# Optimization experiments

Measured on AMD Instinct MI355X. Metric: run time of the kernel, lower is better.

The kernel has to match this reference:

```python
import jax, jax.numpy as jnp
import numpy as np

B, S, D, H = 4, 2048, 2048, 16
DK = D // H

def setup_inputs() -> dict:
    key = jax.random.key(0)
    ks = jax.random.split(key, 9)
    def xavier(k, shape):
        fan_in, fan_out = shape[1], shape[0]
        limit = (6.0 / (fan_in + fan_out)) ** 0.5
        return jax.random.uniform(k, shape, jnp.float32, -limit, limit)
    return {
        "x": jax.random.normal(ks[0], (B, S, D), jnp.float32),
        "Wq": xavier(ks[1], (D, D)), "bq": jnp.zeros((D,), jnp.float32),
        "Wk": xavier(ks[2], (D, D)), "bk": jnp.zeros((D,), jnp.float32),
        "Wv": xavier(ks[3], (D, D)), "bv": jnp.zeros((D,), jnp.float32),
        "Wo": xavier(ks[4], (D, D)), "bo": jnp.zeros((D,), jnp.float32),
    }

def reference(x, Wq, bq, Wk, bk, Wv, bv, Wo, bo):
    b, s, d = x.shape
    scale = DK ** 0.5
    # torch nn.Linear: y = x @ W.T + b
    def proj(W, bias):
        y = jnp.einsum('bsd,ed->bse', x, W) + bias
        return y.reshape(b, s, H, DK).transpose(0, 2, 1, 3)  # (b, h, s, dk)
    Q, K, V = proj(Wq, bq), proj(Wk, bk), proj(Wv, bv)
    scores = jnp.einsum('bhqd,bhkd->bhqk', Q, K) / scale
    causal = jnp.triu(jnp.ones((s, s), dtype=bool), k=1)
    scores = jnp.where(causal[None, None], -jnp.inf, scores)
    attn = jax.nn.softmax(scores, axis=-1)
    ctx = jnp.einsum('bhqk,bhkd->bhqd', attn, V)
    ctx = ctx.transpose(0, 2, 1, 3).reshape(b, s, d)
    out = jnp.einsum('bsd,ed->bse', ctx, Wo) + bo
    return out
```

## Files before the change

kernel.cpp:

```cpp
#include <hip/hip_runtime.h>
#include <hip/hip_bf16.h>
#include <cstdint>

#define B_  4
#define S_  2048
#define D_  2048
#define H_  16
#define DK_ 128

typedef __attribute__((ext_vector_type(8))) short short8;
typedef __attribute__((ext_vector_type(4))) short s16x4;
typedef __attribute__((ext_vector_type(4))) float f32x4;
typedef unsigned short ushort_t;

__device__ __forceinline__ void gl_lds16(const void* g, void* l) {
  __builtin_amdgcn_global_load_lds(
      (const __attribute__((address_space(1))) uint32_t*)g,
      (__attribute__((address_space(3))) uint32_t*)l, 16, 0, 0);
}

__device__ __forceinline__ ushort_t f2bf(float f) {
  __hip_bfloat16 h = __float2bfloat16(f);
  return *(ushort_t*)&h;
}

__global__ __launch_bounds__(256) void cvt_all(
    const float* __restrict__ x,  const float* __restrict__ w0,
    const float* __restrict__ w1, const float* __restrict__ w2,
    const float* __restrict__ w3, ushort_t* __restrict__ dst)
{
  constexpr size_t NE = (size_t)B_ * S_ * D_;
  constexpr size_t NW = (size_t)D_ * D_;
  constexpr int XB = (int)(NE / 8 / 256);
  constexpr int WB = (int)(NW / 8 / 256);

  const int blk = blockIdx.x;
  const float* src;
  size_t base;
  int li;
  if (blk < XB)           { src = x;  base = 0;           li = blk * 256 + threadIdx.x; }
  else if (blk < XB+WB)   { src = w0; base = NE/8;        li = (blk-XB)     * 256 + threadIdx.x; }
  else if (blk < XB+2*WB) { src = w1; base = (NE+NW)/8;   li = (blk-XB-WB)  * 256 + threadIdx.x; }
  else if (blk < XB+3*WB) { src = w2; base = (NE+2*NW)/8; li = (blk-XB-2*WB)* 256 + threadIdx.x; }
  else                    { src = w3; base = (NE+3*NW)/8; li = (blk-XB-3*WB)* 256 + threadIdx.x; }

  float4 a = ((const float4*)src)[li * 2];
  float4 b = ((const float4*)src)[li * 2 + 1];
  short8 o;
  o[0] = (short)f2bf(a.x); o[1] = (short)f2bf(a.y);
  o[2] = (short)f2bf(a.z); o[3] = (short)f2bf(a.w);
  o[4] = (short)f2bf(b.x); o[5] = (short)f2bf(b.y);
  o[6] = (short)f2bf(b.z); o[7] = (short)f2bf(b.w);
  ((short8*)dst)[base + li] = o;
}

#define STAGE_A(q, tt) do {                                                \
    int r0_ = (q) * 64 + w * 8;                                            \
    gl_lds16(Agb + (size_t)(r0_ + lr) * 2048 + (tt) * 64 + lc, &As[r0_ * 64]); \
    r0_ += 128;                                                            \
    gl_lds16(Agb + (size_t)(r0_ + lr) * 2048 + (tt) * 64 + lc, &As[r0_ * 64]); \
  } while (0)
#define STAGE_B(q, tt) do {                                                \
    int r0_ = (w >> 1) * 64 + (q) * 32 + ((w & 1) * 2) * 8;                \
    gl_lds16(Wgb + (size_t)(r0_ + lr) * 2048 + (tt) * 64 + lc, &Bs[r0_ * 64]); \
    r0_ += 8;                                                              \
    gl_lds16(Wgb + (size_t)(r0_ + lr) * 2048 + (tt) * 64 + lc, &Bs[r0_ * 64]); \
  } while (0)

#define GEMM_BODY()                                                               \
  f32x4 acc[8][4] = {};                                                           \
  short8 aA[4][2];                                                                \
  short8 bB[2][2][2];                                                             \
  STAGE_A(0, 0); STAGE_A(1, 0); STAGE_B(0, 0); STAGE_B(1, 0);                     \
  asm volatile("s_waitcnt vmcnt(0)" ::: "memory");                                \
  __builtin_amdgcn_s_barrier();                                                   \
  for (int kt = 0; kt < NT; ++kt) {                                               \
                     \
    _Pragma("unroll")                                                             \
    for (int fm = 0; fm < 4; ++fm)                                                \
      _Pragma("unroll")                                                           \
      for (int kk = 0; kk < 2; ++kk) {                                            \
        const int row = wm * 128 + fm * 16 + l15;                                 \
        aA[fm][kk] = *(const short8*)&As[row * 64 + (((kk * 4 + lhi) ^ (l15 & 7)) << 3)]; \
      }                                                                           \
    _Pragma("unroll")                                                             \
    for (int fn = 0; fn < 2; ++fn)                                                \
      _Pragma("unroll")                                                           \
      for (int kk = 0; kk < 2; ++kk) {                                            \
        const int row = wn * 64 + fn * 16 + l15;                                  \
        bB[0][fn][kk] = *(const short8*)&Bs[row * 64 + (((kk * 4 + lhi) ^ (l15 & 7)) << 3)]; \
      }                                                                           \
    __builtin_amdgcn_s_barrier();                                                 \
    __builtin_amdgcn_s_setprio(1);                                                \
    _Pragma("unroll")                                                             \
    for (int kk = 0; kk < 2; ++kk)                                                \
      _Pragma("unroll")                                                           \
      for (int fm = 0; fm < 4; ++fm)                                              \
        _Pragma("unroll")                                                         \
        for (int fn = 0; fn < 2; ++fn)                                            \
          acc[fm][fn] = __builtin_amdgcn_mfma_f32_16x16x32_bf16(aA[fm][kk], bB[0][fn][kk], acc[fm][fn], 0, 0, 0); \
    __builtin_amdgcn_s_setprio(0);                                                \
    asm volatile("s_waitcnt vmcnt(2)" ::: "memory");           \
    __builtin_amdgcn_s_barrier();                                                 \
         \
    _Pragma("unroll")                                                             \
    for (int fn = 0; fn < 2; ++fn)                                                \
      _Pragma("unroll")                                                           \
      for (int kk = 0; kk < 2; ++kk) {                                            \
        const int row = wn * 64 + 32 + fn * 16 + l15;                             \
        bB[1][fn][kk] = *(const short8*)&Bs[row * 64 + (((kk * 4 + lhi) ^ (l15 & 7)) << 3)]; \
      }                                                                           \
    if (kt + 1 < NT) { STAGE_A(0, kt + 1); STAGE_B(0, kt + 1); }                  \
    __builtin_amdgcn_s_barrier();                                                 \
    __builtin_amdgcn_s_setprio(1);                                                \
    _Pragma("unroll")                                                             \
    for (int kk = 0; kk < 2; ++kk)                                                \
      _Pragma("unroll")                                                           \
      for (int fm = 0; fm < 4; ++fm)                                              \
        _Pragma("unroll")                                                         \
        for (int fn = 0; fn < 2; ++fn)                                            \
          acc[fm][2 + fn] = __builtin_amdgcn_mfma_f32_16x16x32_bf16(aA[fm][kk], bB[1][fn][kk], acc[fm][2 + fn], 0, 0, 0); \
    __builtin_amdgcn_s_setprio(0);                                                \
    if (kt + 1 < NT) { asm volatile("s_waitcnt vmcnt(4)" ::: "memory"); }         \
    else             { asm volatile("s_waitcnt vmcnt(0)" ::: "memory"); }         \
    __builtin_amdgcn_s_barrier();                         \
                   \
    _Pragma("unroll")                                                             \
    for (int fm = 0; fm < 4; ++fm)                                                \
      _Pragma("unroll")                                                           \
      for (int kk = 0; kk < 2; ++kk) {                                            \
        const int row = wm * 128 + 64 + fm * 16 + l15;                            \
        aA[fm][kk] = *(const short8*)&As[row * 64 + (((kk * 4 + lhi) ^ (l15 & 7)) << 3)]; \
      }                                                                           \
    if (kt + 1 < NT) STAGE_B(1, kt + 1);                                          \
    __builtin_amdgcn_s_barrier();                                                 \
    __builtin_amdgcn_s_setprio(1);                                                \
    _Pragma("unroll")                                                             \
    for (int kk = 0; kk < 2; ++kk)                                                \
      _Pragma("unroll")                                                           \
      for (int fm = 0; fm < 4; ++fm)                                              \
        _Pragma("unroll")                                                         \
        for (int fn = 0; fn < 2; ++fn)                                            \
          acc[4 + fm][fn] = __builtin_amdgcn_mfma_f32_16x16x32_bf16(aA[fm][kk], bB[0][fn][kk], acc[4 + fm][fn], 0, 0, 0); \
    __builtin_amdgcn_s_setprio(0);                                                \
    __builtin_amdgcn_s_barrier();                                                 \
                               \
    if (kt + 1 < NT) STAGE_A(1, kt + 1);                                          \
    __builtin_amdgcn_s_setprio(1);                                                \
    _Pragma("unroll")                                                             \
    for (int kk = 0; kk < 2; ++kk)                                                \
      _Pragma("unroll")                                                           \
      for (int fm = 0; fm < 4; ++fm)                                              \
        _Pragma("unroll")                                                         \
        for (int fn = 0; fn < 2; ++fn)                                            \
          acc[4 + fm][2 + fn] = __builtin_amdgcn_mfma_f32_16x16x32_bf16(aA[fm][kk], bB[1][fn][kk], acc[4 + fm][2 + fn], 0, 0, 0); \
    __builtin_amdgcn_s_setprio(0);                                                \
    if (kt + 1 < NT) { asm volatile("s_waitcnt vmcnt(4)" ::: "memory"); }         \
    else             { asm volatile("s_waitcnt vmcnt(0)" ::: "memory"); }         \
    __builtin_amdgcn_s_barrier();                     \
  }

__global__ __launch_bounds__(512, 2) void gemmQKV(
    const ushort_t* __restrict__ A,
    const ushort_t* __restrict__ Wqm, const ushort_t* __restrict__ Wkm,
    const ushort_t* __restrict__ Wvm,
    const float* __restrict__ bq, const float* __restrict__ bk,
    const float* __restrict__ bv,
    ushort_t* __restrict__ Qo, ushort_t* __restrict__ Ko,
    ushort_t* __restrict__ Vo)
{
  constexpr int NT = D_ / 64;

  __shared__ ushort_t As[256 * 64];
  __shared__ ushort_t Bs[256 * 64];

  const int bid = blockIdx.x;
  const int c = bid & 7;
  const int j = bid >> 3;
  const int proj = j >> 5;
  const int s = j & 31;
  const int tnl = s & 7;
  const int tm = c * 4 + (s >> 3);

  const ushort_t* Wsel = (proj == 0) ? Wqm : (proj == 1) ? Wkm : Wvm;
  const float*    bsel = (proj == 0) ? bq  : (proj == 1) ? bk  : bv;
  ushort_t*       osel = (proj == 0) ? Qo  : (proj == 1) ? Ko  : Vo;

  const int t = threadIdx.x;
  const int l = t & 63;
  const int w = t >> 6;
  const int wm = w >> 2;
  const int wn = w & 3;
  const int l15 = l & 15, lhi = l >> 4;
  const int lr = l >> 3;
  const int lc = ((l & 7) ^ lr) * 8;

  const ushort_t* Agb = A + (size_t)(tm * 256) * 2048;
  const ushort_t* Wgb = Wsel + (size_t)(tnl * 256) * 2048;

  GEMM_BODY()

#pragma unroll
  for (int qn = 0; qn < 2; ++qn)
#pragma unroll
    for (int fn = 0; fn < 2; ++fn) {
      const int e = tnl * 256 + wn * 64 + qn * 32 + fn * 16 + l15;
      const float bvv = bsel[e];
      const int h = e >> 7, dk = e & (DK_ - 1);
#pragma unroll
      for (int qm = 0; qm < 2; ++qm)
#pragma unroll
        for (int fm = 0; fm < 4; ++fm) {
          const int srow0 = tm * 256 + wm * 128 + qm * 64 + fm * 16 + lhi * 4;
          const f32x4 v4 = acc[qm * 4 + fm][qn * 2 + fn];
          if (proj == 2) {
            const int b = srow0 >> 11, s0 = srow0 & (S_ - 1);
            s16x4 pk;
#pragma unroll
            for (int r = 0; r < 4; ++r) pk[r] = (short)f2bf(v4[r] + bvv);
            *(s16x4*)(osel + (((size_t)b * H_ + h) * DK_ + dk) * S_ + s0) = pk;
          } else {
#pragma unroll
            for (int r = 0; r < 4; ++r) {
              const int sg = srow0 + r;
              const int b = sg >> 11, sR = sg & (S_ - 1);
              osel[(((size_t)b * H_ + h) * S_ + sR) * DK_ + dk] = f2bf(v4[r] + bvv);
            }
          }
        }
    }
}

__global__ __launch_bounds__(512, 2) void gemmOut(
    const ushort_t* __restrict__ A,
    const ushort_t* __restrict__ W,
    const float* __restrict__ bias,
    float* __restrict__ outp)
{
  constexpr int NT = D_ / 64;
  constexpr int NWG = (B_ * S_ / 256) * (D_ / 256);

  __shared__ ushort_t As[256 * 64];
  __shared__ ushort_t Bs[256 * 64];

  const int bid = blockIdx.x;
  const int swz = (bid & 7) * (NWG / 8) + (bid >> 3);
  const int tm = swz >> 3;
  const int tn = swz & 7;

  const int t = threadIdx.x;
  const int l = t & 63;
  const int w = t >> 6;
  const int wm = w >> 2;
  const int wn = w & 3;
  const int l15 = l & 15, lhi = l >> 4;
  const int lr = l >> 3;
  const int lc = ((l & 7) ^ lr) * 8;

  const ushort_t* Agb = A + (size_t)(tm * 256) * 2048;
  const ushort_t* Wgb = W + (size_t)(tn * 256) * 2048;

  GEMM_BODY()

#pragma unroll
  for (int qn = 0; qn < 2; ++qn)
#pragma unroll
    for (int fn = 0; fn < 2; ++fn) {
      const int e = tn * 256 + wn * 64 + qn * 32 + fn * 16 + l15;
      const float bvv = bias[e];
#pragma unroll
      for (int qm = 0; qm < 2; ++qm)
#pragma unroll
        for (int fm = 0; fm < 4; ++fm) {
          const int srow0 = tm * 256 + wm * 128 + qm * 64 + fm * 16 + lhi * 4;
          const f32x4 v4 = acc[qm * 4 + fm][qn * 2 + fn];
#pragma unroll
          for (int r = 0; r < 4; ++r)
            outp[(size_t)(srow0 + r) * D_ + e] = v4[r] + bvv;
        }
    }
}
#undef STAGE_A
#undef STAGE_B
#undef GEMM_BODY

__global__ __launch_bounds__(256, 2) void attn_kern(
    const ushort_t* __restrict__ Q,
    const ushort_t* __restrict__ K,
    const ushort_t* __restrict__ Vt,
    ushort_t* __restrict__ C)
{
  __shared__ ushort_t Ks[2][64 * 128];
  __shared__ ushort_t Vs[2][128 * 64];
  __shared__ ushort_t Pl[4][32 * 64];

  const int bid = blockIdx.x;
  const int i = bid >> 3;
  const int bh = (bid & 7) * 8 + (i >> 3);
  const int qp = i & 7;

  const ushort_t* Qg = Q + (size_t)bh * S_ * DK_;
  const ushort_t* Kg = K + (size_t)bh * S_ * DK_;
  const ushort_t* Vg = Vt + (size_t)bh * DK_ * S_;
  const int b = bh >> 4, h = bh & 15;

  const int t = threadIdx.x;
  const int l = t & 63;
  const int w = t >> 6;
  const int l15 = l & 15, lhi = l >> 4;

  const float cs = 0.08838834764831845f * 1.4426950408889634f;
  const float DEFER_RAW = 8.0f / cs;

  short8 ones;
#pragma unroll
  for (int j = 0; j < 8; ++j) ones[j] = (short)0x3F80;

  int koff[4], voff[4];
#pragma unroll
  for (int j = 0; j < 4; ++j) {
    const int krow = w * 16 + j * 4 + lhi;
    koff[j] = krow * DK_ + 8 * (l15 ^ ((j * 4 + lhi) & 7));
    const int vrow = (w * 4 + j) * 8 + (l >> 3);
    voff[j] = vrow * S_ + 8 * ((l & 7) ^ (l >> 3));
  }
  int kcol[4];
#pragma unroll
  for (int kt = 0; kt < 4; ++kt)
    kcol[kt] = ((kt * 64 + lhi * 16) ^ ((l15 & 7) << 4)) >> 1;
  int vcol[2];
#pragma unroll
  for (int hb = 0; hb < 2; ++hb)
    vcol[hb] = ((hb * 64 + lhi * 16) ^ ((l15 & 7) << 4)) >> 1;

#define STAGE_KV(pb, kvv) do {                                              \
    _Pragma("unroll")                                                       \
    for (int j = 0; j < 4; ++j) {                                           \
      gl_lds16(Kg + (size_t)(kvv) * DK_ + koff[j], Ks[pb] + (w * 4 + j) * 512); \
      gl_lds16(Vg + (size_t)(kvv) + voff[j],       Vs[pb] + (w * 4 + j) * 512); \
    }                                                                       \
  } while (0)

  for (int pass = 0; pass < 2; ++pass) {
    const int qb = pass ? (15 - qp) : qp;
    const int qrow0 = qb * 128 + w * 32;
    const int nkv = 2 * (qb + 1);

    short8 qa[2][4];
#pragma unroll
    for (int rf = 0; rf < 2; ++rf)
#pragma unroll
      for (int kt = 0; kt < 4; ++kt)
        qa[rf][kt] = *(const short8*)(Qg + (size_t)(qrow0 + rf * 16 + l15) * DK_ + kt * 32 + lhi * 8);

    f32x4 o[2][8] = {};
    f32x4 lsum[2] = {};
    float mrow[2][4];
#pragma unroll
    for (int rf = 0; rf < 2; ++rf)
#pragma unroll
      for (int r = 0; r < 4; ++r) mrow[rf][r] = -1e30f;

    STAGE_KV(0, 0);
    asm volatile("s_waitcnt vmcnt(0)" ::: "memory");
    __syncthreads();

    for (int kvt = 0; kvt < nkv; ++kvt) {
      const int kv = kvt * 64;
      const int p = kvt & 1;

      if (kvt + 1 < nkv) STAGE_KV(p ^ 1, kv + 64);

      f32x4 sf[2][4] = {};
      __builtin_amdgcn_s_setprio(1);
#pragma unroll
      for (int f = 0; f < 4; ++f) {
#pragma unroll
        for (int kt = 0; kt < 4; ++kt) {
          short8 kb = *(const short8*)(Ks[p] + (f * 16 + l15) * 128 + kcol[kt]);
          sf[0][f] = __builtin_amdgcn_mfma_f32_16x16x32_bf16(qa[0][kt], kb, sf[0][f], 0, 0, 0);
          sf[1][f] = __builtin_amdgcn_mfma_f32_16x16x32_bf16(qa[1][kt], kb, sf[1][f], 0, 0, 0);
        }
      }
      __builtin_amdgcn_s_setprio(0);

      float pmax[2][4];
#pragma unroll
      for (int rf = 0; rf < 2; ++rf)
#pragma unroll
        for (int r = 0; r < 4; ++r) pmax[rf][r] = -1e30f;
      const bool domask = (kv + 63 > qrow0);
      if (domask) {
#pragma unroll
        for (int f = 0; f < 4; ++f) {
          const int col = kv + f * 16 + l15;
#pragma unroll
          for (int rf = 0; rf < 2; ++rf)
#pragma unroll
            for (int r = 0; r < 4; ++r) {
              const int row = qrow0 + rf * 16 + lhi * 4 + r;
              if (col > row) sf[rf][f][r] = -1e30f;
              pmax[rf][r] = fmaxf(pmax[rf][r], sf[rf][f][r]);
            }
        }
      } else {
#pragma unroll
        for (int f = 0; f < 4; ++f)
#pragma unroll
          for (int rf = 0; rf < 2; ++rf)
#pragma unroll
            for (int r = 0; r < 4; ++r)
              pmax[rf][r] = fmaxf(pmax[rf][r], sf[rf][f][r]);
      }
#pragma unroll
      for (int d = 1; d < 16; d <<= 1)
#pragma unroll
        for (int rf = 0; rf < 2; ++rf)
#pragma unroll
          for (int r = 0; r < 4; ++r)
            pmax[rf][r] = fmaxf(pmax[rf][r], __shfl_xor(pmax[rf][r], d, 64));

      bool need = false;
#pragma unroll
      for (int rf = 0; rf < 2; ++rf)
#pragma unroll
        for (int r = 0; r < 4; ++r) need |= (pmax[rf][r] > mrow[rf][r] + DEFER_RAW);
      if (__any(need)) {
#pragma unroll
        for (int rf = 0; rf < 2; ++rf)
#pragma unroll
          for (int r = 0; r < 4; ++r) {
            const float mn = fmaxf(mrow[rf][r], pmax[rf][r]);
            const float alpha = __builtin_amdgcn_exp2f((mrow[rf][r] - mn) * cs);
            mrow[rf][r] = mn;
            lsum[rf][r] *= alpha;
#pragma unroll
            for (int n = 0; n < 8; ++n) o[rf][n][r] *= alpha;
          }
      }

      ushort_t* P = Pl[w];
#pragma unroll
      for (int f = 0; f < 4; ++f)
#pragma unroll
        for (int rf = 0; rf < 2; ++rf)
#pragma unroll
          for (int r = 0; r < 4; ++r) {
            const float pv = __builtin_amdgcn_exp2f((sf[rf][f][r] - mrow[rf][r]) * cs);
            const int prow = rf * 16 + lhi * 4 + r;
            P[prow * 64 + ((f * 16 + l15) ^ ((prow & 7) << 3))] = f2bf(pv);
          }

      asm volatile("s_waitcnt lgkmcnt(0)" ::: "memory");
      short8 pa[2][2];
#pragma unroll
      for (int rf = 0; rf < 2; ++rf)
#pragma unroll
        for (int ks = 0; ks < 2; ++ks) {
          const int prow = rf * 16 + l15;
          pa[rf][ks] = *(const short8*)(P + prow * 64 + ((ks * 32 + lhi * 8) ^ ((prow & 7) << 3)));
        }

      __builtin_amdgcn_s_setprio(1);
#pragma unroll
      for (int rf = 0; rf < 2; ++rf) {
        lsum[rf] = __builtin_amdgcn_mfma_f32_16x16x32_bf16(pa[rf][0], ones, lsum[rf], 0, 0, 0);
        lsum[rf] = __builtin_amdgcn_mfma_f32_16x16x32_bf16(pa[rf][1], ones, lsum[rf], 0, 0, 0);
      }
#pragma unroll
      for (int n = 0; n < 8; ++n) {
#pragma unroll
        for (int hb = 0; hb < 2; ++hb) {
          short8 vb = *(const short8*)(Vs[p] + (n * 16 + l15) * 64 + vcol[hb]);
          o[0][n] = __builtin_amdgcn_mfma_f32_16x16x32_bf16(pa[0][hb], vb, o[0][n], 0, 0, 0);
          o[1][n] = __builtin_amdgcn_mfma_f32_16x16x32_bf16(pa[1][hb], vb, o[1][n], 0, 0, 0);
        }
      }
      __builtin_amdgcn_s_setprio(0);

      asm volatile("s_waitcnt vmcnt(0)" ::: "memory");
      __syncthreads();
    }

#pragma unroll
    for (int rf = 0; rf < 2; ++rf) {
      float linv[4];
#pragma unroll
      for (int r = 0; r < 4; ++r) linv[r] = 1.0f / lsum[rf][r];
#pragma unroll
      for (int n = 0; n < 8; ++n) {
        const int dk = n * 16 + l15;
#pragma unroll
        for (int r = 0; r < 4; ++r) {
          const int srow = qrow0 + rf * 16 + lhi * 4 + r;
          C[(((size_t)b * S_ + srow) * H_ + h) * DK_ + dk] = f2bf(o[rf][n][r] * linv[r]);
        }
      }
    }
  }
#undef STAGE_KV
}

extern "C" void kernel_launch(void* const* d_in, const int* in_sizes, int n_in,
                              void* d_out, int out_size, void* d_ws, size_t ws_size,
                              hipStream_t stream) {
  const float* x  = (const float*)d_in[0];
  const float* Wq = (const float*)d_in[1];
  const float* bq = (const float*)d_in[2];
  const float* Wk = (const float*)d_in[3];
  const float* bk = (const float*)d_in[4];
  const float* Wv = (const float*)d_in[5];
  const float* bv = (const float*)d_in[6];
  const float* Wo = (const float*)d_in[7];
  const float* bo = (const float*)d_in[8];
  float* out = (float*)d_out;

  ushort_t* ws = (ushort_t*)d_ws;
  const size_t NE = (size_t)B_ * S_ * D_;
  const size_t NW = (size_t)D_ * D_;
  ushort_t* xb  = ws;
  ushort_t* Wqb = ws + NE;
  ushort_t* Wkb = Wqb + NW;
  ushort_t* Wvb = Wkb + NW;
  ushort_t* Wob = Wvb + NW;
  ushort_t* Qw  = Wob + NW;
  ushort_t* Kw  = Qw + NE;
  ushort_t* Vw  = Kw + NE;
  ushort_t* Cw  = xb;

  const int XB = (int)(NE / 8 / 256);
  const int WB = (int)(NW / 8 / 256);
  cvt_all<<<dim3(XB + 4 * WB), dim3(256), 0, stream>>>(x, Wq, Wk, Wv, Wo, ws);

  gemmQKV<<<dim3(768), dim3(512), 0, stream>>>(xb, Wqb, Wkb, Wvb, bq, bk, bv, Qw, Kw, Vw);
  attn_kern<<<dim3(512), dim3(256), 0, stream>>>(Qw, Kw, Vw, Cw);
  gemmOut<<<dim3(256), dim3(512), 0, stream>>>(Cw, Wob, bo, out);
}
```

Baseline: 412.9 us.

## Double-buffer LDS tiles in QKV and output GEMMs with deeper prefetch

```diff
diff --git a/kernel.cpp b/kernel.cpp
--- a/kernel.cpp
+++ b/kernel.cpp
@@ -54,110 +54,120 @@
   ((short8*)dst)[base + li] = o;
 }
 
-#define STAGE_A(q, tt) do {                                                \
+#define STAGE_A(d, q, tt) do {                                             \
     int r0_ = (q) * 64 + w * 8;                                            \
-    gl_lds16(Agb + (size_t)(r0_ + lr) * 2048 + (tt) * 64 + lc, &As[r0_ * 64]); \
+    gl_lds16(Agb + (size_t)(r0_ + lr) * 2048 + (tt) * 64 + lc, &As[d][r0_ * 64]); \
     r0_ += 128;                                                            \
-    gl_lds16(Agb + (size_t)(r0_ + lr) * 2048 + (tt) * 64 + lc, &As[r0_ * 64]); \
+    gl_lds16(Agb + (size_t)(r0_ + lr) * 2048 + (tt) * 64 + lc, &As[d][r0_ * 64]); \
   } while (0)
-#define STAGE_B(q, tt) do {                                                \
+#define STAGE_B(d, q, tt) do {                                             \
     int r0_ = (w >> 1) * 64 + (q) * 32 + ((w & 1) * 2) * 8;                \
-    gl_lds16(Wgb + (size_t)(r0_ + lr) * 2048 + (tt) * 64 + lc, &Bs[r0_ * 64]); \
+    gl_lds16(Wgb + (size_t)(r0_ + lr) * 2048 + (tt) * 64 + lc, &Bs[d][r0_ * 64]); \
     r0_ += 8;                                                              \
-    gl_lds16(Wgb + (size_t)(r0_ + lr) * 2048 + (tt) * 64 + lc, &Bs[r0_ * 64]); \
+    gl_lds16(Wgb + (size_t)(r0_ + lr) * 2048 + (tt) * 64 + lc, &Bs[d][r0_ * 64]); \
   } while (0)
 
-#define GEMM_BODY()                                                               \
-  f32x4 acc[8][4] = {};                                                           \
-  short8 aA[4][2];                                                                \
-  short8 bB[2][2][2];                                                             \
-  STAGE_A(0, 0); STAGE_A(1, 0); STAGE_B(0, 0); STAGE_B(1, 0);                     \
-  asm volatile("s_waitcnt vmcnt(0)" ::: "memory");                                \
-  __builtin_amdgcn_s_barrier();                                                   \
-  for (int kt = 0; kt < NT; ++kt) {                                               \
-                     \
-    _Pragma("unroll")                                                             \
-    for (int fm = 0; fm < 4; ++fm)                                                \
-      _Pragma("unroll")                                                           \
-      for (int kk = 0; kk < 2; ++kk) {                                            \
-        const int row = wm * 128 + fm * 16 + l15;                                 \
-        aA[fm][kk] = *(const short8*)&As[row * 64 + (((kk * 4 + lhi) ^ (l15 & 7)) << 3)]; \
-      }                                                                           \
-    _Pragma("unroll")                                                             \
-    for (int fn = 0; fn < 2; ++fn)                                                \
-      _Pragma("unroll")                                                           \
-      for (int kk = 0; kk < 2; ++kk) {                                            \
-        const int row = wn * 64 + fn * 16 + l15;                                  \
-        bB[0][fn][kk] = *(const short8*)&Bs[row * 64 + (((kk * 4 + lhi) ^ (l15 & 7)) << 3)]; \
-      }                                                                           \
-    __builtin_amdgcn_s_barrier();                                                 \
-    __builtin_amdgcn_s_setprio(1);                                                \
-    _Pragma("unroll")                                                             \
-    for (int kk = 0; kk < 2; ++kk)                                                \
-      _Pragma("unroll")                                                           \
-      for (int fm = 0; fm < 4; ++fm)                                              \
-        _Pragma("unroll")                                                         \
-        for (int fn = 0; fn < 2; ++fn)                                            \
-          acc[fm][fn] = __builtin_amdgcn_mfma_f32_16x16x32_bf16(aA[fm][kk], bB[0][fn][kk], acc[fm][fn], 0, 0, 0); \
-    __builtin_amdgcn_s_setprio(0);                                                \
-    asm volatile("s_waitcnt vmcnt(2)" ::: "memory");           \
-    __builtin_amdgcn_s_barrier();                                                 \
-         \
-    _Pragma("unroll")                                                             \
-    for (int fn = 0; fn < 2; ++fn)                                                \
-      _Pragma("unroll")                                                           \
-      for (int kk = 0; kk < 2; ++kk) {                                            \
-        const int row = wn * 64 + 32 + fn * 16 + l15;                             \
-        bB[1][fn][kk] = *(const short8*)&Bs[row * 64 + (((kk * 4 + lhi) ^ (l15 & 7)) << 3)]; \
-      }                                                                           \
-    if (kt + 1 < NT) { STAGE_A(0, kt + 1); STAGE_B(0, kt + 1); }                  \
-    __builtin_amdgcn_s_barrier();                                                 \
-    __builtin_amdgcn_s_setprio(1);                                                \
-    _Pragma("unroll")                                                             \
-    for (int kk = 0; kk < 2; ++kk)                                                \
-      _Pragma("unroll")                                                           \
-      for (int fm = 0; fm < 4; ++fm)                                              \
-        _Pragma("unroll")                                                         \
-        for (int fn = 0; fn < 2; ++fn)                                            \
-          acc[fm][2 + fn] = __builtin_amdgcn_mfma_f32_16x16x32_bf16(aA[fm][kk], bB[1][fn][kk], acc[fm][2 + fn], 0, 0, 0); \
-    __builtin_amdgcn_s_setprio(0);                                                \
-    if (kt + 1 < NT) { asm volatile("s_waitcnt vmcnt(4)" ::: "memory"); }         \
-    else             { asm volatile("s_waitcnt vmcnt(0)" ::: "memory"); }         \
-    __builtin_amdgcn_s_barrier();                         \
-                   \
-    _Pragma("unroll")                                                             \
-    for (int fm = 0; fm < 4; ++fm)                                                \
-      _Pragma("unroll")                                                           \
-      for (int kk = 0; kk < 2; ++kk) {                                            \
-        const int row = wm * 128 + 64 + fm * 16 + l15;                            \
-        aA[fm][kk] = *(const short8*)&As[row * 64 + (((kk * 4 + lhi) ^ (l15 & 7)) << 3)]; \
-      }                                                                           \
-    if (kt + 1 < NT) STAGE_B(1, kt + 1);                                          \
-    __builtin_amdgcn_s_barrier();                                                 \
-    __builtin_amdgcn_s_setprio(1);                                                \
-    _Pragma("unroll")                                                             \
-    for (int kk = 0; kk < 2; ++kk)                                                \
-      _Pragma("unroll")                                                           \
-      for (int fm = 0; fm < 4; ++fm)                                              \
-        _Pragma("unroll")                                                         \
-        for (int fn = 0; fn < 2; ++fn)                                            \
-          acc[4 + fm][fn] = __builtin_amdgcn_mfma_f32_16x16x32_bf16(aA[fm][kk], bB[0][fn][kk], acc[4 + fm][fn], 0, 0, 0); \
-    __builtin_amdgcn_s_setprio(0);                                                \
-    __builtin_amdgcn_s_barrier();                                                 \
-                               \
-    if (kt + 1 < NT) STAGE_A(1, kt + 1);                                          \
-    __builtin_amdgcn_s_setprio(1);                                                \
-    _Pragma("unroll")                                                             \
-    for (int kk = 0; kk < 2; ++kk)                                                \
-      _Pragma("unroll")                                                           \
-      for (int fm = 0; fm < 4; ++fm)                                              \
-        _Pragma("unroll")                                                         \
-        for (int fn = 0; fn < 2; ++fn)                                            \
-          acc[4 + fm][2 + fn] = __builtin_amdgcn_mfma_f32_16x16x32_bf16(aA[fm][kk], bB[1][fn][kk], acc[4 + fm][2 + fn], 0, 0, 0); \
-    __builtin_amdgcn_s_setprio(0);                                                \
-    if (kt + 1 < NT) { asm volatile("s_waitcnt vmcnt(4)" ::: "memory"); }         \
-    else             { asm volatile("s_waitcnt vmcnt(0)" ::: "memory"); }         \
-    __builtin_amdgcn_s_barrier();                     \
+#define LDA_Q(d, qm) do {                                                  \
+    _Pragma("unroll")                                                      \
+    for (int fm = 0; fm < 4; ++fm)                                         \
+      _Pragma("unroll")                                                    \
+      for (int kk = 0; kk < 2; ++kk) {                                     \
+        const int row = wm * 128 + (qm) * 64 + fm * 16 + l15;              \
+        aA[fm][kk] = *(const short8*)&As[d][row * 64 + (((kk * 4 + lhi) ^ (l15 & 7)) << 3)]; \
+      }                                                                    \
+  } while (0)
+
+#define LDB_Q(d, bi, qn) do {                                              \
+    _Pragma("unroll")                                                      \
+    for (int fn = 0; fn < 2; ++fn)                                         \
+      _Pragma("unroll")                                                    \
+      for (int kk = 0; kk < 2; ++kk) {                                     \
+        const int row = wn * 64 + (qn) * 32 + fn * 16 + l15;               \
+        bB[bi][fn][kk] = *(const short8*)&Bs[d][row * 64 + (((kk * 4 + lhi) ^ (l15 & 7)) << 3)]; \
+      }                                                                    \
+  } while (0)
+
+#define MM_Q(am, bi) do {                                                  \
+    __builtin_amdgcn_s_setprio(1);                                         \
+    _Pragma("unroll")                                                      \
+    for (int kk = 0; kk < 2; ++kk)                                         \
+      _Pragma("unroll")                                                    \
+      for (int fm = 0; fm < 4; ++fm)                                       \
+        _Pragma("unroll")                                                  \
+        for (int fn = 0; fn < 2; ++fn)                                     \
+          acc[(am) * 4 + fm][(bi) * 2 + fn] = __builtin_amdgcn_mfma_f32_16x16x32_bf16( \
+              aA[fm][kk], bB[bi][fn][kk], acc[(am) * 4 + fm][(bi) * 2 + fn], 0, 0, 0); \
+    __builtin_amdgcn_s_setprio(0);                                         \
+  } while (0)
+
+#define GEMM_BODY()                                                        \
+  f32x4 acc[8][4] = {};                                                    \
+  short8 aA[4][2];                                                         \
+  short8 bB[2][2][2];                                                      \
+        \
+  STAGE_A(0, 0, 0); STAGE_B(0, 0, 0); STAGE_B(0, 1, 0); STAGE_A(0, 1, 0);  \
+  STAGE_A(1, 0, 1); STAGE_B(1, 0, 1); STAGE_B(1, 1, 1);                    \
+  asm volatile("s_waitcnt vmcnt(10)" ::: "memory");                        \
+  __builtin_amdgcn_s_barrier();                                            \
+  for (int j = 0; j < NJ; ++j) {                                           \
+    const int u = 2 * j;                                                   \
+    const bool stg = (j + 1 < NJ);                                         \
+                      \
+    LDA_Q(0, 0); LDB_Q(0, 0, 0);                                           \
+    STAGE_A(1, 1, u + 1);                                                  \
+    __builtin_amdgcn_s_barrier();                                          \
+    MM_Q(0, 0);                                                            \
+    asm volatile("s_waitcnt vmcnt(10)" ::: "memory");                      \
+    __builtin_amdgcn_s_barrier();                                          \
+                                            \
+    LDB_Q(0, 1, 1);                                                        \
+    if (stg) STAGE_A(0, 0, u + 2);                                         \
+    __builtin_amdgcn_s_barrier();                                          \
+    MM_Q(0, 1);                                                            \
+    if (stg) { asm volatile("s_waitcnt vmcnt(10)" ::: "memory"); }         \
+    else     { asm volatile("s_waitcnt vmcnt(8)"  ::: "memory"); }         \
+    __builtin_amdgcn_s_barrier();                                          \
+                                            \
+    LDA_Q(0, 1);                                                           \
+    if (stg) STAGE_B(0, 0, u + 2);                                         \
+    __builtin_amdgcn_s_barrier();                                          \
+    MM_Q(1, 0);                                                            \
+    __builtin_amdgcn_s_barrier();                                          \
+                                            \
+    if (stg) STAGE_B(0, 1, u + 2);                                         \
+    __builtin_amdgcn_s_barrier();                                          \
+    MM_Q(1, 1);                                                            \
+    if (stg) { asm volatile("s_waitcnt vmcnt(10)" ::: "memory"); }         \
+    else     { asm volatile("s_waitcnt vmcnt(4)"  ::: "memory"); }         \
+    __builtin_amdgcn_s_barrier();                                          \
+                                \
+    LDA_Q(1, 0); LDB_Q(1, 0, 0);                                           \
+    if (stg) STAGE_A(0, 1, u + 2);                                         \
+    __builtin_amdgcn_s_barrier();                                          \
+    MM_Q(0, 0);                                                            \
+    if (stg) { asm volatile("s_waitcnt vmcnt(10)" ::: "memory"); }         \
+    else     { asm volatile("s_waitcnt vmcnt(2)"  ::: "memory"); }         \
+    __builtin_amdgcn_s_barrier();                                          \
+                                            \
+    LDB_Q(1, 1, 1);                                                        \
+    if (stg) STAGE_A(1, 0, u + 3);                                         \
+    __builtin_amdgcn_s_barrier();                                          \
+    MM_Q(0, 1);                                                            \
+    if (stg) { asm volatile("s_waitcnt vmcnt(10)" ::: "memory"); }         \
+    else     { asm volatile("s_waitcnt vmcnt(0)"  ::: "memory"); }         \
+    __builtin_amdgcn_s_barrier();                                          \
+                                            \
+    LDA_Q(1, 1);                                                           \
+    if (stg) STAGE_B(1, 0, u + 3);                                         \
+    __builtin_amdgcn_s_barrier();                                          \
+    MM_Q(1, 0);                                                            \
+    __builtin_amdgcn_s_barrier();                                          \
+                                            \
+    if (stg) STAGE_B(1, 1, u + 3);                                         \
+    __builtin_amdgcn_s_barrier();                                          \
+    MM_Q(1, 1);                                                            \
+    if (stg) { asm volatile("s_waitcnt vmcnt(10)" ::: "memory"); }         \
+    __builtin_amdgcn_s_barrier();                                          \
   }
 
 __global__ __launch_bounds__(512, 2) void gemmQKV(
@@ -169,16 +179,16 @@
     ushort_t* __restrict__ Qo, ushort_t* __restrict__ Ko,
     ushort_t* __restrict__ Vo)
 {
-  constexpr int NT = D_ / 64;
-
-  __shared__ ushort_t As[256 * 64];
-  __shared__ ushort_t Bs[256 * 64];
+  constexpr int NJ = (D_ / 64) / 2;
+
+  __shared__ ushort_t As[2][256 * 64];
+  __shared__ ushort_t Bs[2][256 * 64];
 
   const int bid = blockIdx.x;
   const int c = bid & 7;
-  const int j = bid >> 3;
-  const int proj = j >> 5;
-  const int s = j & 31;
+  const int j0 = bid >> 3;
+  const int proj = j0 >> 5;
+  const int s = j0 & 31;
   const int tnl = s & 7;
   const int tm = c * 4 + (s >> 3);
 
@@ -237,11 +247,11 @@
     const float* __restrict__ bias,
     float* __restrict__ outp)
 {
-  constexpr int NT = D_ / 64;
+  constexpr int NJ = (D_ / 64) / 2;
   constexpr int NWG = (B_ * S_ / 256) * (D_ / 256);
 
-  __shared__ ushort_t As[256 * 64];
-  __shared__ ushort_t Bs[256 * 64];
+  __shared__ ushort_t As[2][256 * 64];
+  __shared__ ushort_t Bs[2][256 * 64];
 
   const int bid = blockIdx.x;
   const int swz = (bid & 7) * (NWG / 8) + (bid >> 3);
@@ -282,6 +292,9 @@
 }
 #undef STAGE_A
 #undef STAGE_B
+#undef LDA_Q
+#undef LDB_Q
+#undef MM_Q
 #undef GEMM_BODY
 
 __global__ __launch_bounds__(256, 2) void attn_kern(
```

Measured after the change: 447.9 us. +8.5%, slower.
